# Kernel optimization log

Hardware: AMD Instinct MI355X
Metric: run time of the kernel (lower is better)

The kernel has to match this reference:

```python
import jax, jax.numpy as jnp
import numpy as np

B, T, D, U = 32, 2048, 128, 128


def setup_inputs() -> dict:
    key = jax.random.key(0)
    k1, k2, k3, k4 = jax.random.split(key, 4)
    x = jax.random.normal(k1, (B, T, D), dtype=jnp.float32)
    W_x = jax.random.normal(k2, (D, 4 * U), dtype=jnp.float32) * 0.05
    W_h = jax.random.normal(k3, (U, 4 * U), dtype=jnp.float32) * 0.05
    bias = jax.random.normal(k4, (4 * U,), dtype=jnp.float32) * 0.05
    return {"x": x, "W_x": W_x, "W_h": W_h, "bias": bias}


def reference(x, W_x, W_h, bias):
    # Keras gate order in the packed 4U dim: i, f, c(g), o
    u = W_h.shape[0]
    batch = x.shape[0]
    h0 = jnp.zeros((batch, u), dtype=x.dtype)
    c0 = jnp.zeros((batch, u), dtype=x.dtype)

    def step(carry, x_t):
        h, c = carry
        z = x_t @ W_x + h @ W_h + bias  # [B, 4U], fused 4-gate GEMM
        i = jax.nn.sigmoid(z[:, :u])
        f = jax.nn.sigmoid(z[:, u:2 * u])
        g = jnp.tanh(z[:, 2 * u:3 * u])
        o = jax.nn.sigmoid(z[:, 3 * u:])
        c_new = i * g + f * c
        h_new = o * jnp.tanh(c_new)
        return (h_new, c_new), h_new

    # scan over time: x -> [T, B, D]
    _, hs = jax.lax.scan(step, (h0, c0), jnp.swapaxes(x, 0, 1))
    return hs  # [T, B, U], matches original's np.array(h_sequences)
```

## Files before the change

kernel.cpp:

```cpp
#include <hip/hip_runtime.h>
#include <cstdint>
#include <cstddef>

#define B_ 32
#define T_ 2048
#define D_ 128
#define U_ 128
#define G4_ 512
#define P1_ROWS 32

typedef _Float16 f16x8 __attribute__((ext_vector_type(8)));
typedef float f32x4 __attribute__((ext_vector_type(4)));

__device__ __forceinline__ float sigf(float z) {
  return __builtin_amdgcn_rcpf(1.f + __expf(-z));
}
__device__ __forceinline__ float tanhf_(float z) {
  return 2.f * __builtin_amdgcn_rcpf(1.f + __expf(-2.f * z)) - 1.f;
}

__device__ __forceinline__ void lds_barrier() {
  __builtin_amdgcn_sched_barrier(0);
  asm volatile("s_waitcnt lgkmcnt(0)");
  __builtin_amdgcn_sched_barrier(0);
  __builtin_amdgcn_s_barrier();
  __builtin_amdgcn_sched_barrier(0);
}

__global__ __launch_bounds__(512)
void zx_kernel(const float* __restrict__ x, const float* __restrict__ Wx,
               const float* __restrict__ bias, float* __restrict__ Zx,
               int tbase, int ct) {
  const int j = threadIdx.x;
  const int nt = ct / P1_ROWS;
  const int tblk = blockIdx.x % nt;
  const int b = blockIdx.x / nt;
  const int t0 = tblk * P1_ROWS;

  __shared__ float xsT[D_ * P1_ROWS];

  const float* xp = x + ((size_t)b * T_ + tbase + t0) * D_;
  {
    int e = j * 8;
    int r = e >> 7;
    int k = e & 127;
    float4 v0 = *(const float4*)(xp + e);
    float4 v1 = *(const float4*)(xp + e + 4);
    xsT[(k + 0) * P1_ROWS + r] = v0.x;
    xsT[(k + 1) * P1_ROWS + r] = v0.y;
    xsT[(k + 2) * P1_ROWS + r] = v0.z;
    xsT[(k + 3) * P1_ROWS + r] = v0.w;
    xsT[(k + 4) * P1_ROWS + r] = v1.x;
    xsT[(k + 5) * P1_ROWS + r] = v1.y;
    xsT[(k + 6) * P1_ROWS + r] = v1.z;
    xsT[(k + 7) * P1_ROWS + r] = v1.w;
  }
  __syncthreads();

  const float bj = bias[j];
  float acc[P1_ROWS];
#pragma unroll
  for (int r = 0; r < P1_ROWS; ++r) acc[r] = bj;

  const float* wp = Wx + j;
  float w = wp[0];
#pragma unroll 2
  for (int k = 0; k < D_; ++k) {
    float wn = (k + 1 < D_) ? wp[(size_t)(k + 1) * G4_] : 0.f;
    const float4* xr = (const float4*)(xsT + k * P1_ROWS);
#pragma unroll
    for (int r4 = 0; r4 < P1_ROWS / 4; ++r4) {
      float4 xv = xr[r4];
      acc[4 * r4 + 0] += xv.x * w;
      acc[4 * r4 + 1] += xv.y * w;
      acc[4 * r4 + 2] += xv.z * w;
      acc[4 * r4 + 3] += xv.w * w;
    }
    w = wn;
  }

  float* zp = Zx + ((size_t)b * G4_ + j) * ct + t0;
#pragma unroll
  for (int q = 0; q < P1_ROWS / 4; ++q)
    ((float4*)zp)[q] = make_float4(acc[4 * q], acc[4 * q + 1], acc[4 * q + 2], acc[4 * q + 3]);
}

__global__ __launch_bounds__(512)
void lstm_kernel(const float* __restrict__ Zx, const float* __restrict__ Wh,
                 float* __restrict__ out, float* __restrict__ state,
                 int tbase, int ct, int first) {
  const int j = threadIdx.x;
  const int b = blockIdx.x;
  const int w = j >> 6;
  const int lane = j & 63;
  const int l4 = lane & 15;
  const int kg = lane >> 4;
  const int u = w * 16 + l4;

  f16x8 bf[4][4];
#pragma unroll
  for (int g = 0; g < 4; ++g)
#pragma unroll
    for (int kt = 0; kt < 4; ++kt) {
      f16x8 v;
#pragma unroll
      for (int e = 0; e < 8; ++e)
        v[e] = (_Float16)Wh[(size_t)(kt * 32 + kg * 8 + e) * G4_ + g * U_ + u];
      bf[g][kt] = v;
    }

  __shared__ alignas(16) _Float16 hbuf[2][U_];

  float c_state = 0.f, h0 = 0.f;
  if (!first) {
    h0 = state[b * 2 * U_ + u];
    c_state = state[b * 2 * U_ + U_ + u];
  }
  if (kg == 0) hbuf[0][u] = (_Float16)h0;
  __syncthreads();

  const float4* zq0 = (const float4*)(Zx + ((size_t)b * G4_ + 0 * U_ + u) * ct);
  const float4* zq1 = (const float4*)(Zx + ((size_t)b * G4_ + 1 * U_ + u) * ct);
  const float4* zq2 = (const float4*)(Zx + ((size_t)b * G4_ + 2 * U_ + u) * ct);
  const float4* zq3 = (const float4*)(Zx + ((size_t)b * G4_ + 3 * U_ + u) * ct);

  float4 zc0 = zq0[0], zc1 = zq1[0], zc2 = zq2[0], zc3 = zq3[0];
  float hlast = h0;
  float* outp = out + ((size_t)tbase * B_ + b) * U_ + u;

  for (int tt = 0; tt < ct; tt += 4) {
    float4 zn0, zn1, zn2, zn3;
    if (tt + 4 < ct) {
      const int nq = (tt >> 2) + 1;
      zn0 = zq0[nq]; zn1 = zq1[nq]; zn2 = zq2[nq]; zn3 = zq3[nq];
    } else {
      zn0 = zn1 = zn2 = zn3 = make_float4(0.f, 0.f, 0.f, 0.f);
    }
#pragma unroll
    for (int s = 0; s < 4; ++s) {
      const int t = tt + s;
      const int cur = t & 1;
      const float zi0 = (s == 0) ? zc0.x : (s == 1) ? zc0.y : (s == 2) ? zc0.z : zc0.w;
      const float zi1 = (s == 0) ? zc1.x : (s == 1) ? zc1.y : (s == 2) ? zc1.z : zc1.w;
      const float zi2 = (s == 0) ? zc2.x : (s == 1) ? zc2.y : (s == 2) ? zc2.z : zc2.w;
      const float zi3 = (s == 0) ? zc3.x : (s == 1) ? zc3.y : (s == 2) ? zc3.z : zc3.w;

      const f16x8* hp = (const f16x8*)hbuf[cur];
      f16x8 a0 = hp[0 * 4 + kg];
      f16x8 a1 = hp[1 * 4 + kg];
      f16x8 a2 = hp[2 * 4 + kg];
      f16x8 a3 = hp[3 * 4 + kg];

      f32x4 acc0 = {zi0, zi0, zi0, zi0};
      f32x4 acc1 = {zi1, zi1, zi1, zi1};
      f32x4 acc2 = {zi2, zi2, zi2, zi2};
      f32x4 acc3 = {zi3, zi3, zi3, zi3};
      acc0 = __builtin_amdgcn_mfma_f32_16x16x32_f16(a0, bf[0][0], acc0, 0, 0, 0);
      acc1 = __builtin_amdgcn_mfma_f32_16x16x32_f16(a0, bf[1][0], acc1, 0, 0, 0);
      acc2 = __builtin_amdgcn_mfma_f32_16x16x32_f16(a0, bf[2][0], acc2, 0, 0, 0);
      acc3 = __builtin_amdgcn_mfma_f32_16x16x32_f16(a0, bf[3][0], acc3, 0, 0, 0);
      acc0 = __builtin_amdgcn_mfma_f32_16x16x32_f16(a1, bf[0][1], acc0, 0, 0, 0);
      acc1 = __builtin_amdgcn_mfma_f32_16x16x32_f16(a1, bf[1][1], acc1, 0, 0, 0);
      acc2 = __builtin_amdgcn_mfma_f32_16x16x32_f16(a1, bf[2][1], acc2, 0, 0, 0);
      acc3 = __builtin_amdgcn_mfma_f32_16x16x32_f16(a1, bf[3][1], acc3, 0, 0, 0);
      acc0 = __builtin_amdgcn_mfma_f32_16x16x32_f16(a2, bf[0][2], acc0, 0, 0, 0);
      acc1 = __builtin_amdgcn_mfma_f32_16x16x32_f16(a2, bf[1][2], acc1, 0, 0, 0);
      acc2 = __builtin_amdgcn_mfma_f32_16x16x32_f16(a2, bf[2][2], acc2, 0, 0, 0);
      acc3 = __builtin_amdgcn_mfma_f32_16x16x32_f16(a2, bf[3][2], acc3, 0, 0, 0);
      acc0 = __builtin_amdgcn_mfma_f32_16x16x32_f16(a3, bf[0][3], acc0, 0, 0, 0);
      acc1 = __builtin_amdgcn_mfma_f32_16x16x32_f16(a3, bf[1][3], acc1, 0, 0, 0);
      acc2 = __builtin_amdgcn_mfma_f32_16x16x32_f16(a3, bf[2][3], acc2, 0, 0, 0);
      acc3 = __builtin_amdgcn_mfma_f32_16x16x32_f16(a3, bf[3][3], acc3, 0, 0, 0);

      float i_ = sigf(acc0[0]);
      float f_ = sigf(acc1[0]);
      float g_ = tanhf_(acc2[0]);
      float o_ = sigf(acc3[0]);
      c_state = fmaf(f_, c_state, i_ * g_);
      float hn = o_ * tanhf_(c_state);
      hlast = hn;

      if (kg == 0) {
        outp[(size_t)t * B_ * U_] = hn;
        hbuf[cur ^ 1][u] = (_Float16)hn;
      }
      lds_barrier();
    }
    zc0 = zn0; zc1 = zn1; zc2 = zn2; zc3 = zn3;
  }

  if (kg == 0) {
    state[b * 2 * U_ + u] = hlast;
    state[b * 2 * U_ + U_ + u] = c_state;
  }
}

extern "C" void kernel_launch(void* const* d_in, const int* in_sizes, int n_in,
                              void* d_out, int out_size, void* d_ws, size_t ws_size,
                              hipStream_t stream) {
  const float* x = (const float*)d_in[0];
  const float* Wx = (const float*)d_in[1];
  const float* Wh = (const float*)d_in[2];
  const float* bias = (const float*)d_in[3];
  float* out = (float*)d_out;

  float* state = (float*)d_ws;
  float* zx = (float*)((char*)d_ws + 32768);
  size_t avail = ws_size > 32768 ? ws_size - 32768 : 0;
  size_t per_t = (size_t)B_ * G4_ * sizeof(float);
  long maxct = (long)(avail / per_t);
  int ct;
  if (maxct >= T_) ct = T_;
  else {
    ct = (int)((maxct / P1_ROWS) * P1_ROWS);
    if (ct < P1_ROWS) ct = P1_ROWS;
  }

  for (int tb = 0; tb < T_; tb += ct) {
    int cur = (T_ - tb < ct) ? (T_ - tb) : ct;
    zx_kernel<<<dim3(B_ * (cur / P1_ROWS)), 512, 0, stream>>>(x, Wx, bias, zx, tb, cur);
    lstm_kernel<<<dim3(B_), 512, 0, stream>>>(zx, Wh, out, state, tb, cur, tb == 0 ? 1 : 0);
  }
}
```

Before: 1.166 ms.

## Spread gate activations across lane groups and prescale preactivations by log2e

Gate preactivations are prescaled by -log2(e) (or -2·log2(e) for the tanh gate) in both the input projection and the recurrent weights, so each activation becomes a single exp2 plus reciprocal. Each 16-lane group now evaluates only one gate, and the four gate values are exchanged through two ds_bpermute shuffles with f16 packing instead of every lane computing all four. MFMAs now start from zero and their partial sums are added afterwards, which lets them issue independently. This cuts per-step transcendental work and Zx loads per lane, but adds cross-lane shuffle latency and rounds the gate values to f16, which lowers precision.

```diff
diff --git a/kernel.cpp b/kernel.cpp
--- a/kernel.cpp
+++ b/kernel.cpp
@@ -8,16 +8,11 @@
 #define U_ 128
 #define G4_ 512
 #define P1_ROWS 32
+#define L2E_ 1.4426950408889634f
 
 typedef _Float16 f16x8 __attribute__((ext_vector_type(8)));
+typedef _Float16 f16x2 __attribute__((ext_vector_type(2)));
 typedef float f32x4 __attribute__((ext_vector_type(4)));
-
-__device__ __forceinline__ float sigf(float z) {
-  return __builtin_amdgcn_rcpf(1.f + __expf(-z));
-}
-__device__ __forceinline__ float tanhf_(float z) {
-  return 2.f * __builtin_amdgcn_rcpf(1.f + __expf(-2.f * z)) - 1.f;
-}
 
 __device__ __forceinline__ void lds_barrier() {
   __builtin_amdgcn_sched_barrier(0);
@@ -36,6 +31,7 @@
   const int tblk = blockIdx.x % nt;
   const int b = blockIdx.x / nt;
   const int t0 = tblk * P1_ROWS;
+  const float sj = ((j >> 7) == 2) ? (-2.f * L2E_) : (-L2E_);
 
   __shared__ float xsT[D_ * P1_ROWS];
 
@@ -82,7 +78,8 @@
   float* zp = Zx + ((size_t)b * G4_ + j) * ct + t0;
 #pragma unroll
   for (int q = 0; q < P1_ROWS / 4; ++q)
-    ((float4*)zp)[q] = make_float4(acc[4 * q], acc[4 * q + 1], acc[4 * q + 2], acc[4 * q + 3]);
+    ((float4*)zp)[q] = make_float4(sj * acc[4 * q], sj * acc[4 * q + 1],
+                                   sj * acc[4 * q + 2], sj * acc[4 * q + 3]);
 }
 
 __global__ __launch_bounds__(512)
@@ -97,17 +94,26 @@
   const int kg = lane >> 4;
   const int u = w * 16 + l4;
 
+  const bool evn = (kg & 1) == 0;
+  const bool lowg = kg < 2;
+  const int idx16 = (lane ^ 16) << 2;
+  const int idx32 = (lane ^ 32) << 2;
+  const float mk = (kg == 2) ? 2.f : 1.f;
+  const float bk = (kg == 2) ? -1.f : 0.f;
+
   f16x8 bf[4][4];
 #pragma unroll
-  for (int g = 0; g < 4; ++g)
+  for (int g = 0; g < 4; ++g) {
+    const float sg = (g == 2) ? (-2.f * L2E_) : (-L2E_);
 #pragma unroll
     for (int kt = 0; kt < 4; ++kt) {
       f16x8 v;
 #pragma unroll
       for (int e = 0; e < 8; ++e)
-        v[e] = (_Float16)Wh[(size_t)(kt * 32 + kg * 8 + e) * G4_ + g * U_ + u];
+        v[e] = (_Float16)(sg * Wh[(size_t)(kt * 32 + kg * 8 + e) * G4_ + g * U_ + u]);
       bf[g][kt] = v;
     }
+  }
 
   __shared__ alignas(16) _Float16 hbuf[2][U_];
 
@@ -119,31 +125,20 @@
   if (kg == 0) hbuf[0][u] = (_Float16)h0;
   __syncthreads();
 
-  const float4* zq0 = (const float4*)(Zx + ((size_t)b * G4_ + 0 * U_ + u) * ct);
-  const float4* zq1 = (const float4*)(Zx + ((size_t)b * G4_ + 1 * U_ + u) * ct);
-  const float4* zq2 = (const float4*)(Zx + ((size_t)b * G4_ + 2 * U_ + u) * ct);
-  const float4* zq3 = (const float4*)(Zx + ((size_t)b * G4_ + 3 * U_ + u) * ct);
-
-  float4 zc0 = zq0[0], zc1 = zq1[0], zc2 = zq2[0], zc3 = zq3[0];
+  const float4* zq = (const float4*)(Zx + ((size_t)b * G4_ + kg * U_ + u) * ct);
+  float4 zc = zq[0];
   float hlast = h0;
   float* outp = out + ((size_t)tbase * B_ + b) * U_ + u;
 
+  const f32x4 zero4 = {0.f, 0.f, 0.f, 0.f};
+
   for (int tt = 0; tt < ct; tt += 4) {
-    float4 zn0, zn1, zn2, zn3;
-    if (tt + 4 < ct) {
-      const int nq = (tt >> 2) + 1;
-      zn0 = zq0[nq]; zn1 = zq1[nq]; zn2 = zq2[nq]; zn3 = zq3[nq];
-    } else {
-      zn0 = zn1 = zn2 = zn3 = make_float4(0.f, 0.f, 0.f, 0.f);
-    }
+    float4 zn = (tt + 4 < ct) ? zq[(tt >> 2) + 1] : make_float4(0.f, 0.f, 0.f, 0.f);
 #pragma unroll
     for (int s = 0; s < 4; ++s) {
       const int t = tt + s;
       const int cur = t & 1;
-      const float zi0 = (s == 0) ? zc0.x : (s == 1) ? zc0.y : (s == 2) ? zc0.z : zc0.w;
-      const float zi1 = (s == 0) ? zc1.x : (s == 1) ? zc1.y : (s == 2) ? zc1.z : zc1.w;
-      const float zi2 = (s == 0) ? zc2.x : (s == 1) ? zc2.y : (s == 2) ? zc2.z : zc2.w;
-      const float zi3 = (s == 0) ? zc3.x : (s == 1) ? zc3.y : (s == 2) ? zc3.z : zc3.w;
+      const float zi = (s == 0) ? zc.x : (s == 1) ? zc.y : (s == 2) ? zc.z : zc.w;
 
       const f16x8* hp = (const f16x8*)hbuf[cur];
       f16x8 a0 = hp[0 * 4 + kg];
@@ -151,33 +146,50 @@
       f16x8 a2 = hp[2 * 4 + kg];
       f16x8 a3 = hp[3 * 4 + kg];
 
-      f32x4 acc0 = {zi0, zi0, zi0, zi0};
-      f32x4 acc1 = {zi1, zi1, zi1, zi1};
-      f32x4 acc2 = {zi2, zi2, zi2, zi2};
-      f32x4 acc3 = {zi3, zi3, zi3, zi3};
-      acc0 = __builtin_amdgcn_mfma_f32_16x16x32_f16(a0, bf[0][0], acc0, 0, 0, 0);
-      acc1 = __builtin_amdgcn_mfma_f32_16x16x32_f16(a0, bf[1][0], acc1, 0, 0, 0);
-      acc2 = __builtin_amdgcn_mfma_f32_16x16x32_f16(a0, bf[2][0], acc2, 0, 0, 0);
-      acc3 = __builtin_amdgcn_mfma_f32_16x16x32_f16(a0, bf[3][0], acc3, 0, 0, 0);
-      acc0 = __builtin_amdgcn_mfma_f32_16x16x32_f16(a1, bf[0][1], acc0, 0, 0, 0);
-      acc1 = __builtin_amdgcn_mfma_f32_16x16x32_f16(a1, bf[1][1], acc1, 0, 0, 0);
-      acc2 = __builtin_amdgcn_mfma_f32_16x16x32_f16(a1, bf[2][1], acc2, 0, 0, 0);
-      acc3 = __builtin_amdgcn_mfma_f32_16x16x32_f16(a1, bf[3][1], acc3, 0, 0, 0);
-      acc0 = __builtin_amdgcn_mfma_f32_16x16x32_f16(a2, bf[0][2], acc0, 0, 0, 0);
-      acc1 = __builtin_amdgcn_mfma_f32_16x16x32_f16(a2, bf[1][2], acc1, 0, 0, 0);
-      acc2 = __builtin_amdgcn_mfma_f32_16x16x32_f16(a2, bf[2][2], acc2, 0, 0, 0);
-      acc3 = __builtin_amdgcn_mfma_f32_16x16x32_f16(a2, bf[3][2], acc3, 0, 0, 0);
-      acc0 = __builtin_amdgcn_mfma_f32_16x16x32_f16(a3, bf[0][3], acc0, 0, 0, 0);
-      acc1 = __builtin_amdgcn_mfma_f32_16x16x32_f16(a3, bf[1][3], acc1, 0, 0, 0);
-      acc2 = __builtin_amdgcn_mfma_f32_16x16x32_f16(a3, bf[2][3], acc2, 0, 0, 0);
-      acc3 = __builtin_amdgcn_mfma_f32_16x16x32_f16(a3, bf[3][3], acc3, 0, 0, 0);
-
-      float i_ = sigf(acc0[0]);
-      float f_ = sigf(acc1[0]);
-      float g_ = tanhf_(acc2[0]);
-      float o_ = sigf(acc3[0]);
+      f32x4 c00 = __builtin_amdgcn_mfma_f32_16x16x32_f16(a0, bf[0][0], zero4, 0, 0, 0);
+      f32x4 c10 = __builtin_amdgcn_mfma_f32_16x16x32_f16(a0, bf[1][0], zero4, 0, 0, 0);
+      f32x4 c20 = __builtin_amdgcn_mfma_f32_16x16x32_f16(a0, bf[2][0], zero4, 0, 0, 0);
+      f32x4 c30 = __builtin_amdgcn_mfma_f32_16x16x32_f16(a0, bf[3][0], zero4, 0, 0, 0);
+      f32x4 c01 = __builtin_amdgcn_mfma_f32_16x16x32_f16(a1, bf[0][1], zero4, 0, 0, 0);
+      f32x4 c11 = __builtin_amdgcn_mfma_f32_16x16x32_f16(a1, bf[1][1], zero4, 0, 0, 0);
+      f32x4 c21 = __builtin_amdgcn_mfma_f32_16x16x32_f16(a1, bf[2][1], zero4, 0, 0, 0);
+      f32x4 c31 = __builtin_amdgcn_mfma_f32_16x16x32_f16(a1, bf[3][1], zero4, 0, 0, 0);
+      f32x4 c02 = __builtin_amdgcn_mfma_f32_16x16x32_f16(a2, bf[0][2], zero4, 0, 0, 0);
+      f32x4 c12 = __builtin_amdgcn_mfma_f32_16x16x32_f16(a2, bf[1][2], zero4, 0, 0, 0);
+      f32x4 c22 = __builtin_amdgcn_mfma_f32_16x16x32_f16(a2, bf[2][2], zero4, 0, 0, 0);
+      f32x4 c32 = __builtin_amdgcn_mfma_f32_16x16x32_f16(a2, bf[3][2], zero4, 0, 0, 0);
+      f32x4 c03 = __builtin_amdgcn_mfma_f32_16x16x32_f16(a3, bf[0][3], zero4, 0, 0, 0);
+      f32x4 c13 = __builtin_amdgcn_mfma_f32_16x16x32_f16(a3, bf[1][3], zero4, 0, 0, 0);
+      f32x4 c23 = __builtin_amdgcn_mfma_f32_16x16x32_f16(a3, bf[2][3], zero4, 0, 0, 0);
+      f32x4 c33 = __builtin_amdgcn_mfma_f32_16x16x32_f16(a3, bf[3][3], zero4, 0, 0, 0);
+
+      float z0 = (c00[0] + c01[0]) + (c02[0] + c03[0]);
+      float z1 = (c10[0] + c11[0]) + (c12[0] + c13[0]);
+      float z2 = (c20[0] + c21[0]) + (c22[0] + c23[0]);
+      float z3 = (c30[0] + c31[0]) + (c32[0] + c33[0]);
+      float zsel = lowg ? (evn ? z0 : z1) : (evn ? z2 : z3);
+      float zs = zsel + zi;
+
+      float act = fmaf(__builtin_amdgcn_rcpf(1.f + __builtin_amdgcn_exp2f(zs)), mk, bk);
+
+      float prt = __builtin_bit_cast(
+          float, __builtin_amdgcn_ds_bpermute(idx16, __builtin_bit_cast(int, act)));
+      f16x2 spv = __builtin_bit_cast(f16x2, __builtin_amdgcn_cvt_pkrtz(act, prt));
+      int oth = __builtin_amdgcn_ds_bpermute(idx32, __builtin_bit_cast(int, spv));
+      f16x2 opv = __builtin_bit_cast(f16x2, oth);
+
+      float spl = (float)spv[0], sph = (float)spv[1];
+      float opl = (float)opv[0], oph = (float)opv[1];
+      float ifl = lowg ? spl : opl, ifh = lowg ? sph : oph;
+      float gol = lowg ? opl : spl, goh = lowg ? oph : sph;
+      float i_ = evn ? ifl : ifh, f_ = evn ? ifh : ifl;
+      float g_ = evn ? gol : goh, o_ = evn ? goh : gol;
+
       c_state = fmaf(f_, c_state, i_ * g_);
-      float hn = o_ * tanhf_(c_state);
+      float tc = fmaf(
+          __builtin_amdgcn_rcpf(1.f + __builtin_amdgcn_exp2f(-2.f * L2E_ * c_state)),
+          2.f, -1.f);
+      float hn = o_ * tc;
       hlast = hn;
 
       if (kg == 0) {
@@ -186,7 +198,7 @@
       }
       lds_barrier();
     }
-    zc0 = zn0; zc1 = zn1; zc2 = zn2; zc3 = zn3;
+    zc = zn;
   }
 
   if (kg == 0) {
```

After: 1.227 ms. +5.2%, slower.

## Prescale gate weights by -log2e and split MFMA chains into two accumulators

Applied to the files above, without the earlier changes.

Folds the -log2(e) (or -2·log2(e) for the g gate) factor into W_h and into the precomputed input projection. The activations can then call exp2 directly, with no multiply before the exponent. The 16 dependent MFMAs per step are split into two independent K-halves accumulated separately and summed afterward, which shortens the serial MFMA dependency chain on the recurrent critical path. Scaling W_h before the fp16 cast changes rounding slightly, and the split adds a few scalar adds.

```diff
diff --git a/kernel.cpp b/kernel.cpp
--- a/kernel.cpp
+++ b/kernel.cpp
@@ -8,16 +8,10 @@
 #define U_ 128
 #define G4_ 512
 #define P1_ROWS 32
+#define L2E_ 1.4426950408889634f
 
 typedef _Float16 f16x8 __attribute__((ext_vector_type(8)));
 typedef float f32x4 __attribute__((ext_vector_type(4)));
-
-__device__ __forceinline__ float sigf(float z) {
-  return __builtin_amdgcn_rcpf(1.f + __expf(-z));
-}
-__device__ __forceinline__ float tanhf_(float z) {
-  return 2.f * __builtin_amdgcn_rcpf(1.f + __expf(-2.f * z)) - 1.f;
-}
 
 __device__ __forceinline__ void lds_barrier() {
   __builtin_amdgcn_sched_barrier(0);
@@ -36,6 +30,7 @@
   const int tblk = blockIdx.x % nt;
   const int b = blockIdx.x / nt;
   const int t0 = tblk * P1_ROWS;
+  const float sj = ((j >> 7) == 2) ? (-2.f * L2E_) : (-L2E_);
 
   __shared__ float xsT[D_ * P1_ROWS];
 
@@ -82,7 +77,8 @@
   float* zp = Zx + ((size_t)b * G4_ + j) * ct + t0;
 #pragma unroll
   for (int q = 0; q < P1_ROWS / 4; ++q)
-    ((float4*)zp)[q] = make_float4(acc[4 * q], acc[4 * q + 1], acc[4 * q + 2], acc[4 * q + 3]);
+    ((float4*)zp)[q] = make_float4(sj * acc[4 * q], sj * acc[4 * q + 1],
+                                   sj * acc[4 * q + 2], sj * acc[4 * q + 3]);
 }
 
 __global__ __launch_bounds__(512)
@@ -99,15 +95,17 @@
 
   f16x8 bf[4][4];
 #pragma unroll
-  for (int g = 0; g < 4; ++g)
+  for (int g = 0; g < 4; ++g) {
+    const float sg = (g == 2) ? (-2.f * L2E_) : (-L2E_);
 #pragma unroll
     for (int kt = 0; kt < 4; ++kt) {
       f16x8 v;
 #pragma unroll
       for (int e = 0; e < 8; ++e)
-        v[e] = (_Float16)Wh[(size_t)(kt * 32 + kg * 8 + e) * G4_ + g * U_ + u];
+        v[e] = (_Float16)(sg * Wh[(size_t)(kt * 32 + kg * 8 + e) * G4_ + g * U_ + u]);
       bf[g][kt] = v;
     }
+  }
 
   __shared__ alignas(16) _Float16 hbuf[2][U_];
 
@@ -127,6 +125,8 @@
   float4 zc0 = zq0[0], zc1 = zq1[0], zc2 = zq2[0], zc3 = zq3[0];
   float hlast = h0;
   float* outp = out + ((size_t)tbase * B_ + b) * U_ + u;
+
+  const f32x4 zero4 = {0.f, 0.f, 0.f, 0.f};
 
   for (int tt = 0; tt < ct; tt += 4) {
     float4 zn0, zn1, zn2, zn3;
@@ -147,37 +147,42 @@
 
       const f16x8* hp = (const f16x8*)hbuf[cur];
       f16x8 a0 = hp[0 * 4 + kg];
+      f16x8 a2 = hp[2 * 4 + kg];
       f16x8 a1 = hp[1 * 4 + kg];
-      f16x8 a2 = hp[2 * 4 + kg];
       f16x8 a3 = hp[3 * 4 + kg];
 
-      f32x4 acc0 = {zi0, zi0, zi0, zi0};
-      f32x4 acc1 = {zi1, zi1, zi1, zi1};
-      f32x4 acc2 = {zi2, zi2, zi2, zi2};
-      f32x4 acc3 = {zi3, zi3, zi3, zi3};
-      acc0 = __builtin_amdgcn_mfma_f32_16x16x32_f16(a0, bf[0][0], acc0, 0, 0, 0);
-      acc1 = __builtin_amdgcn_mfma_f32_16x16x32_f16(a0, bf[1][0], acc1, 0, 0, 0);
-      acc2 = __builtin_amdgcn_mfma_f32_16x16x32_f16(a0, bf[2][0], acc2, 0, 0, 0);
-      acc3 = __builtin_amdgcn_mfma_f32_16x16x32_f16(a0, bf[3][0], acc3, 0, 0, 0);
-      acc0 = __builtin_amdgcn_mfma_f32_16x16x32_f16(a1, bf[0][1], acc0, 0, 0, 0);
-      acc1 = __builtin_amdgcn_mfma_f32_16x16x32_f16(a1, bf[1][1], acc1, 0, 0, 0);
-      acc2 = __builtin_amdgcn_mfma_f32_16x16x32_f16(a1, bf[2][1], acc2, 0, 0, 0);
-      acc3 = __builtin_amdgcn_mfma_f32_16x16x32_f16(a1, bf[3][1], acc3, 0, 0, 0);
-      acc0 = __builtin_amdgcn_mfma_f32_16x16x32_f16(a2, bf[0][2], acc0, 0, 0, 0);
-      acc1 = __builtin_amdgcn_mfma_f32_16x16x32_f16(a2, bf[1][2], acc1, 0, 0, 0);
-      acc2 = __builtin_amdgcn_mfma_f32_16x16x32_f16(a2, bf[2][2], acc2, 0, 0, 0);
-      acc3 = __builtin_amdgcn_mfma_f32_16x16x32_f16(a2, bf[3][2], acc3, 0, 0, 0);
-      acc0 = __builtin_amdgcn_mfma_f32_16x16x32_f16(a3, bf[0][3], acc0, 0, 0, 0);
-      acc1 = __builtin_amdgcn_mfma_f32_16x16x32_f16(a3, bf[1][3], acc1, 0, 0, 0);
-      acc2 = __builtin_amdgcn_mfma_f32_16x16x32_f16(a3, bf[2][3], acc2, 0, 0, 0);
-      acc3 = __builtin_amdgcn_mfma_f32_16x16x32_f16(a3, bf[3][3], acc3, 0, 0, 0);
-
-      float i_ = sigf(acc0[0]);
-      float f_ = sigf(acc1[0]);
-      float g_ = tanhf_(acc2[0]);
-      float o_ = sigf(acc3[0]);
+      f32x4 aA0 = __builtin_amdgcn_mfma_f32_16x16x32_f16(a0, bf[0][0], zero4, 0, 0, 0);
+      f32x4 aA1 = __builtin_amdgcn_mfma_f32_16x16x32_f16(a0, bf[1][0], zero4, 0, 0, 0);
+      f32x4 aA2 = __builtin_amdgcn_mfma_f32_16x16x32_f16(a0, bf[2][0], zero4, 0, 0, 0);
+      f32x4 aA3 = __builtin_amdgcn_mfma_f32_16x16x32_f16(a0, bf[3][0], zero4, 0, 0, 0);
+      f32x4 aB0 = __builtin_amdgcn_mfma_f32_16x16x32_f16(a2, bf[0][2], zero4, 0, 0, 0);
+      f32x4 aB1 = __builtin_amdgcn_mfma_f32_16x16x32_f16(a2, bf[1][2], zero4, 0, 0, 0);
+      f32x4 aB2 = __builtin_amdgcn_mfma_f32_16x16x32_f16(a2, bf[2][2], zero4, 0, 0, 0);
+      f32x4 aB3 = __builtin_amdgcn_mfma_f32_16x16x32_f16(a2, bf[3][2], zero4, 0, 0, 0);
+      aA0 = __builtin_amdgcn_mfma_f32_16x16x32_f16(a1, bf[0][1], aA0, 0, 0, 0);
+      aA1 = __builtin_amdgcn_mfma_f32_16x16x32_f16(a1, bf[1][1], aA1, 0, 0, 0);
+      aA2 = __builtin_amdgcn_mfma_f32_16x16x32_f16(a1, bf[2][1], aA2, 0, 0, 0);
+      aA3 = __builtin_amdgcn_mfma_f32_16x16x32_f16(a1, bf[3][1], aA3, 0, 0, 0);
+      aB0 = __builtin_amdgcn_mfma_f32_16x16x32_f16(a3, bf[0][3], aB0, 0, 0, 0);
+      aB1 = __builtin_amdgcn_mfma_f32_16x16x32_f16(a3, bf[1][3], aB1, 0, 0, 0);
+      aB2 = __builtin_amdgcn_mfma_f32_16x16x32_f16(a3, bf[2][3], aB2, 0, 0, 0);
+      aB3 = __builtin_amdgcn_mfma_f32_16x16x32_f16(a3, bf[3][3], aB3, 0, 0, 0);
+
+      float zs0 = (aA0[0] + aB0[0]) + zi0;
+      float zs1 = (aA1[0] + aB1[0]) + zi1;
+      float zs2 = (aA2[0] + aB2[0]) + zi2;
+      float zs3 = (aA3[0] + aB3[0]) + zi3;
+
+      float i_ = __builtin_amdgcn_rcpf(1.f + __builtin_amdgcn_exp2f(zs0));
+      float f_ = __builtin_amdgcn_rcpf(1.f + __builtin_amdgcn_exp2f(zs1));
+      float g_ = fmaf(__builtin_amdgcn_rcpf(1.f + __builtin_amdgcn_exp2f(zs2)), 2.f, -1.f);
+      float o_ = __builtin_amdgcn_rcpf(1.f + __builtin_amdgcn_exp2f(zs3));
+
       c_state = fmaf(f_, c_state, i_ * g_);
-      float hn = o_ * tanhf_(c_state);
+      float tc = fmaf(
+          __builtin_amdgcn_rcpf(1.f + __builtin_amdgcn_exp2f(-2.f * L2E_ * c_state)),
+          2.f, -1.f);
+      float hn = o_ * tc;
       hlast = hn;
 
       if (kg == 0) {
```

Measured after the change: 1.383 ms. 1.19x slower.

## Fuse input projection and recurrence into one persistent kernel with flag-based handoff

Applied to the files above, without the earlier changes.

Replaces the two-kernel sequence with a single launch. 32 blocks run the LSTM recurrence while 224 worker blocks compute the x·W_x+bias tiles chunk by chunk and publish per-chunk ready flags through agent-scope atomics. The recurrence blocks spin-wait on each chunk's flag, so the input projection overlaps with the serial recurrence instead of running before it. This relies on all blocks being co-resident to avoid deadlock and adds a memset plus polling overhead. The old two-kernel path is kept as a fallback for small workspaces.

```diff
diff --git a/kernel.cpp b/kernel.cpp
--- a/kernel.cpp
+++ b/kernel.cpp
@@ -8,6 +8,9 @@
 #define U_ 128
 #define G4_ 512
 #define P1_ROWS 32
+#define NW_ 224
+#define CT_ 32
+#define NCH_ (T_ / CT_)
 
 typedef _Float16 f16x8 __attribute__((ext_vector_type(8)));
 typedef float f32x4 __attribute__((ext_vector_type(4)));
@@ -27,19 +30,19 @@
   __builtin_amdgcn_sched_barrier(0);
 }
 
-__global__ __launch_bounds__(512)
-void zx_kernel(const float* __restrict__ x, const float* __restrict__ Wx,
-               const float* __restrict__ bias, float* __restrict__ Zx,
-               int tbase, int ct) {
+__device__ __forceinline__ void wait_chunk(unsigned* f) {
+  while (__hip_atomic_load(f, __ATOMIC_RELAXED, __HIP_MEMORY_SCOPE_AGENT) == 0u)
+    __builtin_amdgcn_s_sleep(2);
+  __builtin_amdgcn_fence(__ATOMIC_ACQUIRE, "agent");
+}
+
+__device__ __forceinline__ void zx_tile(const float* __restrict__ x,
+                                        const float* __restrict__ Wx,
+                                        const float* __restrict__ bias,
+                                        float* __restrict__ Zx, float* xsT,
+                                        int b, int t0, int zstride) {
   const int j = threadIdx.x;
-  const int nt = ct / P1_ROWS;
-  const int tblk = blockIdx.x % nt;
-  const int b = blockIdx.x / nt;
-  const int t0 = tblk * P1_ROWS;
-
-  __shared__ float xsT[D_ * P1_ROWS];
-
-  const float* xp = x + ((size_t)b * T_ + tbase + t0) * D_;
+  const float* xp = x + ((size_t)b * T_ + t0) * D_;
   {
     int e = j * 8;
     int r = e >> 7;
@@ -79,18 +82,38 @@
     w = wn;
   }
 
-  float* zp = Zx + ((size_t)b * G4_ + j) * ct + t0;
+  float* zp = Zx + ((size_t)b * G4_ + j) * zstride + t0;
 #pragma unroll
   for (int q = 0; q < P1_ROWS / 4; ++q)
     ((float4*)zp)[q] = make_float4(acc[4 * q], acc[4 * q + 1], acc[4 * q + 2], acc[4 * q + 3]);
 }
 
 __global__ __launch_bounds__(512)
-void lstm_kernel(const float* __restrict__ Zx, const float* __restrict__ Wh,
-                 float* __restrict__ out, float* __restrict__ state,
-                 int tbase, int ct, int first) {
+void fused_kernel(const float* __restrict__ x, const float* __restrict__ Wx,
+                  const float* __restrict__ Wh, const float* __restrict__ bias,
+                  float* __restrict__ out, float* __restrict__ Zx,
+                  unsigned* __restrict__ flags) {
+  __shared__ float xsT_s[D_ * P1_ROWS];
+  __shared__ alignas(16) _Float16 hbuf[2][U_];
+
+  const int blk = blockIdx.x;
+
+  if (blk >= B_) {
+    for (int tile = blk - B_; tile < NCH_ * B_; tile += NW_) {
+      const int tc = tile >> 5;
+      const int b = tile & (B_ - 1);
+      zx_tile(x, Wx, bias, Zx, xsT_s, b, tc * CT_, T_);
+      __threadfence();
+      __syncthreads();
+      if (threadIdx.x == 0)
+        __hip_atomic_store(&flags[tile], 1u, __ATOMIC_RELEASE, __HIP_MEMORY_SCOPE_AGENT);
+      __syncthreads();
+    }
+    return;
+  }
+
   const int j = threadIdx.x;
-  const int b = blockIdx.x;
+  const int b = blk;
   const int w = j >> 6;
   const int lane = j & 63;
   const int l4 = lane & 15;
@@ -109,28 +132,28 @@
       bf[g][kt] = v;
     }
 
-  __shared__ alignas(16) _Float16 hbuf[2][U_];
-
-  float c_state = 0.f, h0 = 0.f;
-  if (!first) {
-    h0 = state[b * 2 * U_ + u];
-    c_state = state[b * 2 * U_ + U_ + u];
-  }
-  if (kg == 0) hbuf[0][u] = (_Float16)h0;
+  float c_state = 0.f;
+  if (kg == 0) hbuf[0][u] = (_Float16)0.f;
   __syncthreads();
 
-  const float4* zq0 = (const float4*)(Zx + ((size_t)b * G4_ + 0 * U_ + u) * ct);
-  const float4* zq1 = (const float4*)(Zx + ((size_t)b * G4_ + 1 * U_ + u) * ct);
-  const float4* zq2 = (const float4*)(Zx + ((size_t)b * G4_ + 2 * U_ + u) * ct);
-  const float4* zq3 = (const float4*)(Zx + ((size_t)b * G4_ + 3 * U_ + u) * ct);
+  const float4* zq0 = (const float4*)(Zx + ((size_t)b * G4_ + 0 * U_ + u) * T_);
+  const float4* zq1 = (const float4*)(Zx + ((size_t)b * G4_ + 1 * U_ + u) * T_);
+  const float4* zq2 = (const float4*)(Zx + ((size_t)b * G4_ + 2 * U_ + u) * T_);
+  const float4* zq3 = (const float4*)(Zx + ((size_t)b * G4_ + 3 * U_ + u) * T_);
+
+  wait_chunk(&flags[0 * B_ + b]);
+  wait_chunk(&flags[1 * B_ + b]);
 
   float4 zc0 = zq0[0], zc1 = zq1[0], zc2 = zq2[0], zc3 = zq3[0];
-  float hlast = h0;
-  float* outp = out + ((size_t)tbase * B_ + b) * U_ + u;
-
-  for (int tt = 0; tt < ct; tt += 4) {
+  float* outp = out + ((size_t)0 * B_ + b) * U_ + u;
+
+  for (int tt = 0; tt < T_; tt += 4) {
+    if ((tt & (CT_ - 1)) == 0 && tt) {
+      const int tc = tt >> 5;
+      if (tc + 1 < NCH_) wait_chunk(&flags[(tc + 1) * B_ + b]);
+    }
     float4 zn0, zn1, zn2, zn3;
-    if (tt + 4 < ct) {
+    if (tt + 4 < T_) {
       const int nq = (tt >> 2) + 1;
       zn0 = zq0[nq]; zn1 = zq1[nq]; zn2 = zq2[nq]; zn3 = zq3[nq];
     } else {
@@ -178,6 +201,122 @@
       float o_ = sigf(acc3[0]);
       c_state = fmaf(f_, c_state, i_ * g_);
       float hn = o_ * tanhf_(c_state);
+
+      if (kg == 0) {
+        outp[(size_t)t * B_ * U_] = hn;
+        hbuf[cur ^ 1][u] = (_Float16)hn;
+      }
+      lds_barrier();
+    }
+    zc0 = zn0; zc1 = zn1; zc2 = zn2; zc3 = zn3;
+  }
+}
+
+__global__ __launch_bounds__(512)
+void zx_kernel(const float* __restrict__ x, const float* __restrict__ Wx,
+               const float* __restrict__ bias, float* __restrict__ Zx,
+               int tbase, int ct) {
+  __shared__ float xsT[D_ * P1_ROWS];
+  const int nt = ct / P1_ROWS;
+  const int tblk = blockIdx.x % nt;
+  const int b = blockIdx.x / nt;
+  zx_tile(x, Wx, bias, Zx, xsT, b, tblk * P1_ROWS, ct);
+  (void)tbase;
+}
+
+__global__ __launch_bounds__(512)
+void lstm_kernel(const float* __restrict__ Zx, const float* __restrict__ Wh,
+                 float* __restrict__ out, float* __restrict__ state,
+                 int tbase, int ct, int first) {
+  const int j = threadIdx.x;
+  const int b = blockIdx.x;
+  const int w = j >> 6;
+  const int lane = j & 63;
+  const int l4 = lane & 15;
+  const int kg = lane >> 4;
+  const int u = w * 16 + l4;
+
+  f16x8 bf[4][4];
+#pragma unroll
+  for (int g = 0; g < 4; ++g)
+#pragma unroll
+    for (int kt = 0; kt < 4; ++kt) {
+      f16x8 v;
+#pragma unroll
+      for (int e = 0; e < 8; ++e)
+        v[e] = (_Float16)Wh[(size_t)(kt * 32 + kg * 8 + e) * G4_ + g * U_ + u];
+      bf[g][kt] = v;
+    }
+
+  __shared__ alignas(16) _Float16 hbuf[2][U_];
+
+  float c_state = 0.f, h0 = 0.f;
+  if (!first) {
+    h0 = state[b * 2 * U_ + u];
+    c_state = state[b * 2 * U_ + U_ + u];
+  }
+  if (kg == 0) hbuf[0][u] = (_Float16)h0;
+  __syncthreads();
+
+  const float4* zq0 = (const float4*)(Zx + ((size_t)b * G4_ + 0 * U_ + u) * ct);
+  const float4* zq1 = (const float4*)(Zx + ((size_t)b * G4_ + 1 * U_ + u) * ct);
+  const float4* zq2 = (const float4*)(Zx + ((size_t)b * G4_ + 2 * U_ + u) * ct);
+  const float4* zq3 = (const float4*)(Zx + ((size_t)b * G4_ + 3 * U_ + u) * ct);
+
+  float4 zc0 = zq0[0], zc1 = zq1[0], zc2 = zq2[0], zc3 = zq3[0];
+  float hlast = h0;
+  float* outp = out + ((size_t)tbase * B_ + b) * U_ + u;
+
+  for (int tt = 0; tt < ct; tt += 4) {
+    float4 zn0, zn1, zn2, zn3;
+    if (tt + 4 < ct) {
+      const int nq = (tt >> 2) + 1;
+      zn0 = zq0[nq]; zn1 = zq1[nq]; zn2 = zq2[nq]; zn3 = zq3[nq];
+    } else {
+      zn0 = zn1 = zn2 = zn3 = make_float4(0.f, 0.f, 0.f, 0.f);
+    }
+#pragma unroll
+    for (int s = 0; s < 4; ++s) {
+      const int t = tt + s;
+      const int cur = t & 1;
+      const float zi0 = (s == 0) ? zc0.x : (s == 1) ? zc0.y : (s == 2) ? zc0.z : zc0.w;
+      const float zi1 = (s == 0) ? zc1.x : (s == 1) ? zc1.y : (s == 2) ? zc1.z : zc1.w;
+      const float zi2 = (s == 0) ? zc2.x : (s == 1) ? zc2.y : (s == 2) ? zc2.z : zc2.w;
+      const float zi3 = (s == 0) ? zc3.x : (s == 1) ? zc3.y : (s == 2) ? zc3.z : zc3.w;
+
+      const f16x8* hp = (const f16x8*)hbuf[cur];
+      f16x8 a0 = hp[0 * 4 + kg];
+      f16x8 a1 = hp[1 * 4 + kg];
+      f16x8 a2 = hp[2 * 4 + kg];
+      f16x8 a3 = hp[3 * 4 + kg];
+
+      f32x4 acc0 = {zi0, zi0, zi0, zi0};
+      f32x4 acc1 = {zi1, zi1, zi1, zi1};
+      f32x4 acc2 = {zi2, zi2, zi2, zi2};
+      f32x4 acc3 = {zi3, zi3, zi3, zi3};
+      acc0 = __builtin_amdgcn_mfma_f32_16x16x32_f16(a0, bf[0][0], acc0, 0, 0, 0);
+      acc1 = __builtin_amdgcn_mfma_f32_16x16x32_f16(a0, bf[1][0], acc1, 0, 0, 0);
+      acc2 = __builtin_amdgcn_mfma_f32_16x16x32_f16(a0, bf[2][0], acc2, 0, 0, 0);
+      acc3 = __builtin_amdgcn_mfma_f32_16x16x32_f16(a0, bf[3][0], acc3, 0, 0, 0);
+      acc0 = __builtin_amdgcn_mfma_f32_16x16x32_f16(a1, bf[0][1], acc0, 0, 0, 0);
+      acc1 = __builtin_amdgcn_mfma_f32_16x16x32_f16(a1, bf[1][1], acc1, 0, 0, 0);
+      acc2 = __builtin_amdgcn_mfma_f32_16x16x32_f16(a1, bf[2][1], acc2, 0, 0, 0);
+      acc3 = __builtin_amdgcn_mfma_f32_16x16x32_f16(a1, bf[3][1], acc3, 0, 0, 0);
+      acc0 = __builtin_amdgcn_mfma_f32_16x16x32_f16(a2, bf[0][2], acc0, 0, 0, 0);
+      acc1 = __builtin_amdgcn_mfma_f32_16x16x32_f16(a2, bf[1][2], acc1, 0, 0, 0);
+      acc2 = __builtin_amdgcn_mfma_f32_16x16x32_f16(a2, bf[2][2], acc2, 0, 0, 0);
+      acc3 = __builtin_amdgcn_mfma_f32_16x16x32_f16(a2, bf[3][2], acc3, 0, 0, 0);
+      acc0 = __builtin_amdgcn_mfma_f32_16x16x32_f16(a3, bf[0][3], acc0, 0, 0, 0);
+      acc1 = __builtin_amdgcn_mfma_f32_16x16x32_f16(a3, bf[1][3], acc1, 0, 0, 0);
+      acc2 = __builtin_amdgcn_mfma_f32_16x16x32_f16(a3, bf[2][3], acc2, 0, 0, 0);
+      acc3 = __builtin_amdgcn_mfma_f32_16x16x32_f16(a3, bf[3][3], acc3, 0, 0, 0);
+
+      float i_ = sigf(acc0[0]);
+      float f_ = sigf(acc1[0]);
+      float g_ = tanhf_(acc2[0]);
+      float o_ = sigf(acc3[0]);
+      c_state = fmaf(f_, c_state, i_ * g_);
+      float hn = o_ * tanhf_(c_state);
       hlast = hn;
 
       if (kg == 0) {
@@ -204,21 +343,30 @@
   const float* bias = (const float*)d_in[3];
   float* out = (float*)d_out;
 
-  float* state = (float*)d_ws;
+  const size_t zx_bytes = (size_t)B_ * G4_ * T_ * sizeof(float);
   float* zx = (float*)((char*)d_ws + 32768);
-  size_t avail = ws_size > 32768 ? ws_size - 32768 : 0;
-  size_t per_t = (size_t)B_ * G4_ * sizeof(float);
-  long maxct = (long)(avail / per_t);
-  int ct;
-  if (maxct >= T_) ct = T_;
-  else {
-    ct = (int)((maxct / P1_ROWS) * P1_ROWS);
-    if (ct < P1_ROWS) ct = P1_ROWS;
-  }
-
-  for (int tb = 0; tb < T_; tb += ct) {
-    int cur = (T_ - tb < ct) ? (T_ - tb) : ct;
-    zx_kernel<<<dim3(B_ * (cur / P1_ROWS)), 512, 0, stream>>>(x, Wx, bias, zx, tb, cur);
-    lstm_kernel<<<dim3(B_), 512, 0, stream>>>(zx, Wh, out, state, tb, cur, tb == 0 ? 1 : 0);
-  }
-}
+
+  if (ws_size >= 32768 + zx_bytes) {
+    unsigned* flags = (unsigned*)d_ws;
+    hipMemsetAsync(flags, 0, NCH_ * B_ * sizeof(unsigned), stream);
+    fused_kernel<<<dim3(B_ + NW_), 512, 0, stream>>>(x, Wx, Wh, bias, out, zx, flags);
+  } else {
+    float* state = (float*)d_ws;
+    size_t avail = ws_size > 32768 ? ws_size - 32768 : 0;
+    size_t per_t = (size_t)B_ * G4_ * sizeof(float);
+    long maxct = (long)(avail / per_t);
+    int ct;
+    if (maxct >= T_) ct = T_;
+    else {
+      ct = (int)((maxct / P1_ROWS) * P1_ROWS);
+      if (ct < P1_ROWS) ct = P1_ROWS;
+    }
+    for (int tb = 0; tb < T_; tb += ct) {
+      int cur = (T_ - tb < ct) ? (T_ - tb) : ct;
+      zx_kernel<<<dim3(B_ * (cur / P1_ROWS)), 512, 0, stream>>>(
+          x + (size_t)tb * D_, Wx, bias, zx, 0, cur);
+      lstm_kernel<<<dim3(B_), 512, 0, stream>>>(zx, Wh, out, state, tb, cur,
+                                                tb == 0 ? 1 : 0);
+    }
+  }
+}
```

Result: slower. 1.850 ms (+58.6%).
